# Kernel tuning notes

Hardware: AMD Instinct MI355X
Metric: run time of the kernel (lower is better)

The kernel has to match this reference:

```python
import jax, jax.numpy as jnp
import numpy as np

B, T, N, D = 64, 12, 207, 128
H, ORDER = 8, 2
HID = 2 * D  # mlp_ratio = 2


def _ln(x, g, b, eps=1e-5):
    m = x.mean(-1, keepdims=True)
    v = ((x - m) ** 2).mean(-1, keepdims=True)
    return (x - m) * jax.lax.rsqrt(v + eps) * g + b


def _l2norm(t, eps=1e-12):
    # matches torch.nn.functional.normalize(dim=-1)
    n = jnp.sqrt((t * t).sum(-1, keepdims=True))
    return t / jnp.maximum(n, eps)


def _fast_attn(q, k, v):
    # q, k, v: (B2, L, H, Dh); Performer-style linear attention from FastAttentionLayer.fast_attention
    q = _l2norm(q)
    k = _l2norm(k)
    L = q.shape[1]
    kvs = jnp.einsum('blhm,blhd->bhmd', k, v)
    num = jnp.einsum('bnhm,bhmd->bnhd', q, kvs) + L * v
    ks_sum = k.sum(axis=1)  # (B2, H, Dh)
    den = jnp.einsum('bnhm,bhm->bnh', q, ks_sum)[..., None] + L
    return num / jnp.maximum(den, 1e-5)


def _fast_layer(x, qkv_w, out_w, out_b):
    # x: (B, T, N, D). qkv_bias=False (mask arg), kernel=3 -> out_proj: Linear(2D, D)
    b, t, n, d = x.shape
    dh = d // H
    qkv = x @ qkv_w.T  # (B, T, N, 3D)
    q, k, v = jnp.split(qkv, 3, axis=-1)
    # spatial pass: attend over the N nodes for each (b, t)
    out_s = _fast_attn(q.reshape(b * t, n, H, dh),
                       k.reshape(b * t, n, H, dh),
                       v.reshape(b * t, n, H, dh)).reshape(b, t, n, d)
    # temporal pass: attend over the T steps for each (b, n)
    qt = q.transpose(0, 2, 1, 3).reshape(b * n, t, H, dh)
    kt = k.transpose(0, 2, 1, 3).reshape(b * n, t, H, dh)
    vt = v.transpose(0, 2, 1, 3).reshape(b * n, t, H, dh)
    out_t = _fast_attn(qt, kt, vt).reshape(b, n, t, d).transpose(0, 2, 1, 3)
    return jnp.concatenate([out_s, out_t], -1) @ out_w.T + out_b


def _forward(x, graph, qkv_w, out_w, out_b, pw_w, pw_b,
             fc1_w, fc1_b, fc2_w, fc2_b, ln1_g, ln1_b, ln2_g, ln2_b):
    # GraphPropagate: x_list = [x, graph @ x, ...] (Ks = ORDER hops)
    xs = [x]
    xk = x
    for _ in range(ORDER - 1):
        xk = jnp.einsum('thi,btij->bthj', graph, xk)
        xs.append(xk)
    # per-hop fast attention + zero-init pointwise branch, summed over hops
    agg = jnp.zeros_like(x)
    for i in range(ORDER):
        agg = agg + _fast_layer(xs[i], qkv_w[i], out_w[i], out_b[i]) + xs[i] @ pw_w[i].T + pw_b[i]
    h = _ln(x + agg, ln1_g, ln1_b)
    ff = jax.nn.relu(h @ fc1_w.T + fc1_b) @ fc2_w.T + fc2_b
    return _ln(h + ff, ln2_g, ln2_b)


def setup_inputs() -> dict:
    key = jax.random.key(0)
    ks = jax.random.split(key, 8)
    s = 0.02
    return {
        'x': jax.random.normal(ks[0], (B, T, N, D), jnp.float32),
        'graph': jax.random.uniform(ks[1], (T, N, N), jnp.float32) / N,
        'qkv_w': jax.random.normal(ks[2], (ORDER, 3 * D, D), jnp.float32) * s,
        'out_w': jax.random.normal(ks[3], (ORDER, D, 2 * D), jnp.float32) * s,
        'out_b': jnp.zeros((ORDER, D), jnp.float32),
        'pw_w': jax.random.normal(ks[4], (ORDER, D, D), jnp.float32) * s,
        'pw_b': jnp.zeros((ORDER, D), jnp.float32),
        'fc1_w': jax.random.normal(ks[5], (HID, D), jnp.float32) * s,
        'fc1_b': jnp.zeros((HID,), jnp.float32),
        'fc2_w': jax.random.normal(ks[6], (D, HID), jnp.float32) * s,
        'fc2_b': jnp.zeros((D,), jnp.float32),
        'ln1_g': jnp.ones((D,), jnp.float32),
        'ln1_b': jnp.zeros((D,), jnp.float32),
        'ln2_g': jnp.ones((D,), jnp.float32),
        'ln2_b': jnp.zeros((D,), jnp.float32),
    }


def reference(x, graph, qkv_w, out_w, out_b, pw_w, pw_b,
              fc1_w, fc1_b, fc2_w, fc2_b, ln1_g, ln1_b, ln2_g, ln2_b):
    return _forward(x, graph, qkv_w, out_w, out_b, pw_w, pw_b,
                    fc1_w, fc1_b, fc2_w, fc2_b, ln1_g, ln1_b, ln2_g, ln2_b)
```

## Files before the change

kernel.cpp:

```cpp
#include <hip/hip_runtime.h>
#include <hip/hip_bf16.h>

#define BB 64
#define TT 12
#define NN 207
#define DD 128
#define HH 8
#define DH 16
#define MROWS (BB*TT*NN)
#define KPAD 224
#define AW 768
#define CHB 32
#define CROWS (CHB*TT*NN)

typedef __bf16 bf16x8 __attribute__((ext_vector_type(8)));
typedef __bf16 bf16x4 __attribute__((ext_vector_type(4)));
typedef float  f32x4  __attribute__((ext_vector_type(4)));

__device__ inline float  b2f(__bf16 v){ return (float)v; }
__device__ inline __bf16 f2b(float v){ return (__bf16)v; }
__device__ inline bf16x8 ldfrag(const __bf16* p){ return *reinterpret_cast<const bf16x8*>(p); }

__device__ inline void gload_lds16(const __bf16* g, __bf16* l){
    __builtin_amdgcn_global_load_lds(
        (const __attribute__((address_space(1))) void*)(g),
        (__attribute__((address_space(3))) void*)(l), 16, 0, 0);
}
__device__ inline int swz(int r){ return (r ^ (r>>2)) & 3; }

__global__ __launch_bounds__(256) void xcopy_kernel(const float* __restrict__ x, __bf16* __restrict__ abuf)
{
    int nt = gridDim.x*256;
    for (int gIdx = blockIdx.x*256 + threadIdx.x; gIdx < MROWS*16; gIdx += nt) {
        int row = gIdx >> 4, c8 = (gIdx & 15)*8;
        const float* s = x + (size_t)row*DD + c8;
        f32x4 a = *reinterpret_cast<const f32x4*>(s);
        f32x4 b = *reinterpret_cast<const f32x4*>(s+4);
        bf16x8 r;
        #pragma unroll
        for (int i=0;i<4;i++){ r[i] = f2b(a[i]); r[i+4] = f2b(b[i]); }
        *reinterpret_cast<bf16x8*>(abuf + (size_t)row*AW + c8) = r;
    }
}

__global__ __launch_bounds__(256) void prep_misc_kernel(
    const float* __restrict__ graph, const float* __restrict__ qkv_w,
    const float* __restrict__ out_w, const float* __restrict__ out_b,
    const float* __restrict__ pw_w,  const float* __restrict__ pw_b,
    const float* __restrict__ fc1_w, const float* __restrict__ fc2_w,
    __bf16* __restrict__ gpad, __bf16* __restrict__ qkv_wb, __bf16* __restrict__ wcomb,
    __bf16* __restrict__ fc1_wb, __bf16* __restrict__ fc2_wb, float* __restrict__ bias_comb)
{
    int nt = gridDim.x*256;
    int tid = blockIdx.x*256 + threadIdx.x;
    for (int i = tid; i < TT*NN*KPAD; i += nt) {
        int k = i % KPAD, r = i / KPAD;
        gpad[i] = (k < NN) ? f2b(graph[(size_t)r*NN + k]) : f2b(0.f);
    }
    for (int i = tid; i < 2*3*DD*DD; i += nt) qkv_wb[i] = f2b(qkv_w[i]);
    for (int i = tid; i < DD*AW; i += nt) {
        int c = i / AW, j = i % AW;
        float v;
        if      (j < 128) v = pw_w[c*128 + j];
        else if (j < 256) v = pw_w[128*128 + c*128 + (j-128)];
        else if (j < 512) v = out_w[c*256 + (j-256)];
        else              v = out_w[128*256 + c*256 + (j-512)];
        wcomb[i] = f2b(v);
    }
    for (int i = tid; i < 2*DD*DD; i += nt) fc1_wb[i] = f2b(fc1_w[i]);
    for (int i = tid; i < 2*DD*DD; i += nt) fc2_wb[i] = f2b(fc2_w[i]);
    for (int i = tid; i < DD; i += nt)
        bias_comb[i] = pw_b[i] + pw_b[128+i] + out_b[i] + out_b[128+i];
}

__global__ __launch_bounds__(256) void propagate_kernel(const __bf16* __restrict__ gp,
    __bf16* __restrict__ abuf)
{
    int bt   = blockIdx.x;
    int t    = bt % TT;
    int tile = blockIdx.y;
    int lane = threadIdx.x & 63, w = threadIdx.x >> 6;
    int lhi = lane >> 4, llo = lane & 15;
    __shared__ __attribute__((aligned(16))) __bf16 XT[DD][40];
    const __bf16* xbt  = abuf + (size_t)bt*NN*AW;
    const __bf16* grow = gp + (size_t)t*NN*KPAD;
    int rowbase = tile*64 + w*16;
    f32x4 acc[8];
    #pragma unroll
    for (int i=0;i<8;i++) acc[i] = (f32x4){0.f,0.f,0.f,0.f};
    int arow = rowbase + llo; if (arow > NN-1) arow = NN-1;
    for (int k0=0; k0<KPAD; k0+=32) {
        __syncthreads();
        for (int kl = (threadIdx.x>>7); kl < 32; kl += 2) {
            int kk = k0 + kl, c = threadIdx.x & 127;
            XT[c][kl] = (kk < NN) ? xbt[(size_t)kk*AW + c] : f2b(0.f);
        }
        __syncthreads();
        bf16x8 a = ldfrag(grow + (size_t)arow*KPAD + k0 + lhi*8);
        #pragma unroll
        for (int cf=0;cf<8;cf++){
            bf16x8 b = *reinterpret_cast<const bf16x8*>(&XT[cf*16+llo][lhi*8]);
            acc[cf] = __builtin_amdgcn_mfma_f32_16x16x32_bf16(a, b, acc[cf], 0,0,0);
        }
    }
    #pragma unroll
    for (int e=0;e<4;e++){
        int row = rowbase + lhi*4 + e;
        if (row < NN) {
            #pragma unroll
            for (int cf=0;cf<8;cf++)
                abuf[((size_t)bt*NN + row)*AW + DD + cf*16 + llo] = f2b(acc[cf][e]);
        }
    }
}

template<int MODE, bool RELU>
__global__ __launch_bounds__(512) void gemm_kernel(const __bf16* __restrict__ A, size_t lda,
    const __bf16* __restrict__ W, const float* __restrict__ bias,
    void* out, size_t ldc, int K, int mend,
    const __bf16* __restrict__ resid, size_t ldr,
    const float* __restrict__ lng, const float* __restrict__ lnb)
{
    __shared__ __attribute__((aligned(16))) __bf16 lds[3][12288];
    int w = threadIdx.x >> 6, lane = threadIdx.x & 63;
    int lhi = lane >> 4, llo = lane & 15;
    size_t row0 = (size_t)blockIdx.x*256;
    int col0 = blockIdx.y*128;
    int nt = K >> 5;

    int sA0 = (w*2+0)*64 + lane, sA1 = (w*2+1)*64 + lane, sW = w*64 + lane;
    int rA0 = sA0>>2, uA0 = sA0&3, rA1 = sA1>>2, uA1 = sA1&3, rW = sW>>2, uW = sW&3;
    long gr0 = (long)row0 + rA0; if (gr0 >= mend) gr0 = mend-1;
    long gr1 = (long)row0 + rA1; if (gr1 >= mend) gr1 = mend-1;
    const __bf16* gA0 = A + (size_t)gr0*lda + ((uA0 ^ swz(rA0))<<3);
    const __bf16* gA1 = A + (size_t)gr1*lda + ((uA1 ^ swz(rA1))<<3);
    const __bf16* gW  = W + (size_t)(col0 + rW)*K + ((uW ^ swz(rW))<<3);
    __bf16* base0 = &lds[0][0];

    int aoff[2], woff[8];
    #pragma unroll
    for (int rt=0;rt<2;rt++){
        int rl = w*32 + rt*16 + llo;
        aoff[rt] = rl*32 + ((lhi ^ swz(rl))<<3);
    }
    #pragma unroll
    for (int cf=0;cf<8;cf++){
        int wr = cf*16 + llo;
        woff[cf] = 8192 + wr*32 + ((lhi ^ swz(wr))<<3);
    }

    f32x4 acc[2][8];
    #pragma unroll
    for (int i=0;i<2;i++)
        #pragma unroll
        for (int j=0;j<8;j++) acc[i][j] = (f32x4){0.f,0.f,0.f,0.f};

    #define STAGE(buf, tt) { int k0 = (tt)<<5; __bf16* Lw = base0 + (buf)*12288;           \
        gload_lds16(gA0 + k0, Lw + (w*2+0)*512);                                           \
        gload_lds16(gA1 + k0, Lw + (w*2+1)*512);                                           \
        gload_lds16(gW  + k0, Lw + 8192 + w*512); }

    STAGE(0,0); STAGE(1,1); STAGE(2,2);

    int cur = 0;
    for (int t = 0; t < nt; ++t) {
        if (t <= nt-3)      asm volatile("s_waitcnt vmcnt(6)" ::: "memory");
        else if (t == nt-2) asm volatile("s_waitcnt vmcnt(3)" ::: "memory");
        else                asm volatile("s_waitcnt vmcnt(0)" ::: "memory");
        __builtin_amdgcn_s_barrier();
        __builtin_amdgcn_sched_barrier(0);
        const __bf16* Lb = base0 + cur*12288;
        bf16x8 a[2], b[8];
        #pragma unroll
        for (int rt=0;rt<2;rt++) a[rt] = *reinterpret_cast<const bf16x8*>(&Lb[aoff[rt]]);
        #pragma unroll
        for (int cf=0;cf<8;cf++)  b[cf] = *reinterpret_cast<const bf16x8*>(&Lb[woff[cf]]);
        asm volatile("s_waitcnt lgkmcnt(0)" ::: "memory");
        __builtin_amdgcn_sched_barrier(0);
        __builtin_amdgcn_s_barrier();
        if (t+3 < nt) STAGE(cur, t+3);
        #pragma unroll
        for (int rt=0;rt<2;rt++)
            #pragma unroll
            for (int cf=0;cf<8;cf++)
                acc[rt][cf] = __builtin_amdgcn_mfma_f32_16x16x32_bf16(a[rt], b[cf], acc[rt][cf], 0,0,0);
        cur = (cur == 2) ? 0 : cur + 1;
    }
    #undef STAGE

    float bv[8];
    #pragma unroll
    for (int cf=0;cf<8;cf++) bv[cf] = bias ? bias[col0 + cf*16 + llo] : 0.f;

    if (MODE == 0) {
        #pragma unroll
        for (int rt=0;rt<2;rt++) {
            #pragma unroll
            for (int e=0;e<4;e++) {
                size_t row = row0 + (size_t)w*32 + rt*16 + lhi*4 + e;
                if ((long)row >= mend) continue;
                #pragma unroll
                for (int cf=0;cf<8;cf++) {
                    float v = acc[rt][cf][e] + bv[cf];
                    if (RELU) v = fmaxf(v, 0.f);
                    ((__bf16*)out)[row*ldc + col0 + cf*16 + llo] = f2b(v);
                }
            }
        }
    } else {
        float g8[8], b8[8];
        #pragma unroll
        for (int cf=0;cf<8;cf++){ int c = cf*16 + llo; g8[cf] = lng[c]; b8[cf] = lnb[c]; }
        #pragma unroll
        for (int rt=0;rt<2;rt++) {
            #pragma unroll
            for (int e=0;e<4;e++) {
                size_t row = row0 + (size_t)w*32 + rt*16 + lhi*4 + e;
                if ((long)row >= mend) continue;
                float vals[8], s = 0.f, ss = 0.f;
                #pragma unroll
                for (int cf=0;cf<8;cf++) {
                    int c = cf*16 + llo;
                    float r = b2f(resid[row*ldr + c]);
                    float v = acc[rt][cf][e] + bv[cf] + r;
                    vals[cf] = v; s += v; ss += v*v;
                }
                #pragma unroll
                for (int o=1;o<16;o<<=1){ s += __shfl_xor(s,o,64); ss += __shfl_xor(ss,o,64); }
                float mean = s * (1.f/DD);
                float var  = ss * (1.f/DD) - mean*mean;
                float rs   = rsqrtf(var + 1e-5f);
                #pragma unroll
                for (int cf=0;cf<8;cf++) {
                    float v = (vals[cf]-mean)*rs*g8[cf] + b8[cf];
                    size_t idx = row*ldc + cf*16 + llo;
                    if (MODE == 3) ((__bf16*)out)[idx] = f2b(v);
                    else           ((float*)out)[idx]  = v;
                }
            }
        }
    }
}

template<bool RELU>
__global__ __launch_bounds__(256) void sgemm_k128(const __bf16* __restrict__ A, size_t lda,
    const __bf16* __restrict__ W, const float* __restrict__ bias,
    __bf16* __restrict__ out, size_t ldc, int ngroups)
{
    __shared__ __attribute__((aligned(16))) __bf16 lds[12][2048];
    int w = threadIdx.x >> 6, lane = threadIdx.x & 63;
    int lhi = lane >> 4, llo = lane & 15;
    int col0 = blockIdx.y*128;

    bf16x8 wf[4][8];
    #pragma unroll
    for (int ks=0;ks<4;ks++)
        #pragma unroll
        for (int cf=0;cf<8;cf++)
            wf[ks][cf] = ldfrag(W + (size_t)(col0 + cf*16 + llo)*128 + ks*32 + lhi*8);

    f32x4 bvv[8];
    #pragma unroll
    for (int cf=0;cf<8;cf++){
        if (bias) bvv[cf] = *reinterpret_cast<const f32x4*>(bias + col0 + cf*16 + lhi*4);
        else      bvv[cf] = (f32x4){0.f,0.f,0.f,0.f};
    }

    size_t gsrc[4];
    #pragma unroll
    for (int j=0;j<4;j++){
        int r = j*4 + lhi;
        int u = llo ^ r;
        gsrc[j] = (size_t)r*lda + (size_t)u*8;
    }
    int aoff[4];
    #pragma unroll
    for (int ks=0;ks<4;ks++) aoff[ks] = llo*128 + (((ks<<2)|lhi) ^ llo)*8;

    int gw = blockIdx.x*4 + w, stride = gridDim.x*4;
    int n = (gw < ngroups) ? ((ngroups-1-gw)/stride + 1) : 0;
    __bf16* slab0 = &lds[w*3][0];

    #define SSTAGE(i) { size_t rbase = (size_t)(gw + (size_t)(i)*stride)*16*lda;           \
        __bf16* L = slab0 + ((i)%3)*2048;                                                  \
        gload_lds16(A + rbase + gsrc[0], L);                                               \
        gload_lds16(A + rbase + gsrc[1], L + 512);                                         \
        gload_lds16(A + rbase + gsrc[2], L + 1024);                                        \
        gload_lds16(A + rbase + gsrc[3], L + 1536); }

    if (n > 0) SSTAGE(0);
    if (n > 1) SSTAGE(1);

    for (int i = 0; i < n; ++i) {
        int kept = ((i+1 < n) ? 4 : 0) + ((i >= 2) ? 16 : i*8);
        if      (kept >= 20) asm volatile("s_waitcnt vmcnt(20)" ::: "memory");
        else if (kept == 16) asm volatile("s_waitcnt vmcnt(16)" ::: "memory");
        else if (kept == 12) asm volatile("s_waitcnt vmcnt(12)" ::: "memory");
        else if (kept == 8)  asm volatile("s_waitcnt vmcnt(8)"  ::: "memory");
        else if (kept == 4)  asm volatile("s_waitcnt vmcnt(4)"  ::: "memory");
        else                 asm volatile("s_waitcnt vmcnt(0)"  ::: "memory");

        const __bf16* Ls = slab0 + (i%3)*2048;
        bf16x8 a[4];
        #pragma unroll
        for (int ks=0;ks<4;ks++) a[ks] = *reinterpret_cast<const bf16x8*>(&Ls[aoff[ks]]);

        if (i+2 < n) SSTAGE(i+2);

        f32x4 acc[8];
        #pragma unroll
        for (int cf=0;cf<8;cf++) acc[cf] = (f32x4){0.f,0.f,0.f,0.f};
        #pragma unroll
        for (int ks=0;ks<4;ks++)
            #pragma unroll
            for (int cf=0;cf<8;cf++)
                acc[cf] = __builtin_amdgcn_mfma_f32_16x16x32_bf16(wf[ks][cf], a[ks], acc[cf], 0,0,0);

        size_t grow = (size_t)(gw + (size_t)i*stride)*16 + llo;
        #pragma unroll
        for (int cf=0;cf<8;cf++){
            bf16x4 o;
            #pragma unroll
            for (int e=0;e<4;e++){
                float v = acc[cf][e] + bvv[cf][e];
                if (RELU) v = fmaxf(v, 0.f);
                o[e] = f2b(v);
            }
            *reinterpret_cast<bf16x4*>(out + grow*ldc + col0 + cf*16 + lhi*4) = o;
        }
    }
    #undef SSTAGE
}

#define ACH 32
__global__ __launch_bounds__(256) void attn_s_kernel(const __bf16* __restrict__ qkv,
                                                     __bf16* __restrict__ outp)
{
    int bt = blockIdx.x, g = blockIdx.y;
    const __bf16* base = qkv + (size_t)bt*NN*384 + g*32;
    __shared__ __attribute__((aligned(16))) __bf16 qbuf[224][40];
    __shared__ __attribute__((aligned(16))) __bf16 vbuf[224][40];
    __shared__ __attribute__((aligned(16))) __bf16 kbuf[ACH][40];
    __shared__ float flk[4][16][17];
    __shared__ float fls[4][16];
    int tid = threadIdx.x;
    int wave = tid >> 6, lane = tid & 63;
    int h2 = tid >> 7;
    int dd = tid & 15;
    int oct = ((tid >> 4) & 3) | ((wave & 1) << 2);
    float kvs_col[16]; float ks = 0.f;
    #pragma unroll
    for (int m=0;m<16;m++) kvs_col[m] = 0.f;

    for (int c0 = 0; c0 < NN; c0 += ACH) {
        __syncthreads();
        for (int i = tid; i < ACH*12; i += 256) {
            int r = i/12, u = i%12, seg = u>>2, uu = u&3;
            int nn = c0 + r;
            bf16x8 v8 = (bf16x8){};
            if (nn < NN) v8 = *reinterpret_cast<const bf16x8*>(base + (size_t)nn*384 + seg*128 + uu*8);
            if      (seg == 0) *reinterpret_cast<bf16x8*>(&qbuf[nn][uu*8]) = v8;
            else if (seg == 1) *reinterpret_cast<bf16x8*>(&kbuf[r][uu*8])  = v8;
            else               *reinterpret_cast<bf16x8*>(&vbuf[nn][uu*8]) = v8;
        }
        __syncthreads();
        #pragma unroll
        for (int j=0;j<4;j++){
            int r = oct + 8*j; int nn = c0 + r;
            if (nn >= NN) continue;
            bf16x8 k0 = *reinterpret_cast<const bf16x8*>(&kbuf[r][h2*16]);
            bf16x8 k1 = *reinterpret_cast<const bf16x8*>(&kbuf[r][h2*16+8]);
            float sk = 0.f;
            #pragma unroll
            for (int m=0;m<8;m++){
                float a0=b2f(k0[m]), a1=b2f(k1[m]); sk += a0*a0 + a1*a1;
            }
            float iv = 1.f/fmaxf(sqrtf(sk), 1e-12f);
            float vv  = b2f(vbuf[nn][h2*16+dd]);
            float kdd = b2f(kbuf[r][h2*16+dd]);
            float t2 = iv*vv;
            #pragma unroll
            for (int m=0;m<8;m++){
                kvs_col[m]   += b2f(k0[m])*t2;
                kvs_col[m+8] += b2f(k1[m])*t2;
            }
            ks += kdd*iv;
        }
    }
    #pragma unroll
    for (int m=0;m<16;m++){
        kvs_col[m] += __shfl_xor(kvs_col[m], 16, 64);
        kvs_col[m] += __shfl_xor(kvs_col[m], 32, 64);
    }
    ks += __shfl_xor(ks, 16, 64);
    ks += __shfl_xor(ks, 32, 64);
    if (lane < 16){
        #pragma unroll
        for (int m=0;m<16;m++) flk[wave][m][lane] = kvs_col[m];
        fls[wave][lane] = ks;
    }
    __syncthreads();
    float ksr[16];
    #pragma unroll
    for (int m=0;m<16;m++){
        kvs_col[m] += flk[wave^1][m][dd];
        ksr[m] = fls[h2*2][m] + fls[h2*2+1][m];
    }

    for (int nn = oct; nn < NN; nn += 8) {
        bf16x8 q0 = *reinterpret_cast<const bf16x8*>(&qbuf[nn][h2*16]);
        bf16x8 q1 = *reinterpret_cast<const bf16x8*>(&qbuf[nn][h2*16+8]);
        float sq = 0.f, num = 0.f, den = 0.f;
        #pragma unroll
        for (int m=0;m<8;m++){
            float qm0 = b2f(q0[m]), qm1 = b2f(q1[m]);
            sq  += qm0*qm0 + qm1*qm1;
            num += qm0*kvs_col[m] + qm1*kvs_col[m+8];
            den += qm0*ksr[m]     + qm1*ksr[m+8];
        }
        float iq = 1.f/fmaxf(sqrtf(sq), 1e-12f);
        float vv = b2f(vbuf[nn][h2*16+dd]);
        float o = (num*iq + (float)NN*vv) / fmaxf(den*iq + (float)NN, 1e-5f);
        outp[((size_t)bt*NN + nn)*AW + g*32 + h2*16 + dd] = f2b(o);
    }
}

__global__ __launch_bounds__(256) void attn_t_kernel(const __bf16* __restrict__ qkv,
                                                     __bf16* __restrict__ outp)
{
    int b = blockIdx.x;
    int nn0 = blockIdx.y * 2;
    __shared__ __attribute__((aligned(16))) __bf16 rows[TT][2][384];
    __shared__ float invq[2][TT][8], invk2[2][TT][8];
    int tid = threadIdx.x;
    for (int i = tid; i < TT*2*48; i += 256) {
        int t = i / 96, rem = i % 96;
        int nl = rem / 48, g = rem % 48;
        int nn = nn0 + nl;
        bf16x8 v8 = (bf16x8){};
        if (nn < NN) v8 = *reinterpret_cast<const bf16x8*>(qkv + ((size_t)(b*TT+t)*NN + nn)*384 + g*8);
        *reinterpret_cast<bf16x8*>(&rows[t][nl][g*8]) = v8;
    }
    __syncthreads();
    if (tid < 192) {
        int hh = tid & 7, t = (tid >> 3) % TT, nl = tid / 96;
        bf16x8 q0 = *reinterpret_cast<const bf16x8*>(&rows[t][nl][hh*16]);
        bf16x8 q1 = *reinterpret_cast<const bf16x8*>(&rows[t][nl][hh*16+8]);
        bf16x8 k0 = *reinterpret_cast<const bf16x8*>(&rows[t][nl][128+hh*16]);
        bf16x8 k1 = *reinterpret_cast<const bf16x8*>(&rows[t][nl][128+hh*16+8]);
        float sq = 0.f, sk = 0.f;
        #pragma unroll
        for (int m=0;m<8;m++){
            float a0=b2f(q0[m]), a1=b2f(q1[m]); sq += a0*a0 + a1*a1;
            float c0v=b2f(k0[m]), c1=b2f(k1[m]); sk += c0v*c0v + c1*c1;
        }
        invq[nl][t][hh]  = 1.f/fmaxf(sqrtf(sq), 1e-12f);
        invk2[nl][t][hh] = 1.f/fmaxf(sqrtf(sk), 1e-12f);
    }
    __syncthreads();
    int dd = tid & 15, h = (tid >> 4) & 7, nl = tid >> 7;
    int nn = nn0 + nl;
    float kvs_col[16], ksum[16];
    #pragma unroll
    for (int m=0;m<16;m++){ kvs_col[m]=0.f; ksum[m]=0.f; }
    #pragma unroll
    for (int t=0;t<TT;t++){
        float iv = invk2[nl][t][h];
        bf16x8 k0 = *reinterpret_cast<const bf16x8*>(&rows[t][nl][128+h*16]);
        bf16x8 k1 = *reinterpret_cast<const bf16x8*>(&rows[t][nl][128+h*16+8]);
        float vv = b2f(rows[t][nl][256+h*16+dd]);
        float t2 = iv*vv;
        #pragma unroll
        for (int m=0;m<8;m++){
            float km0 = b2f(k0[m]), km1 = b2f(k1[m]);
            kvs_col[m]   += km0*t2;  ksum[m]   += km0*iv;
            kvs_col[m+8] += km1*t2;  ksum[m+8] += km1*iv;
        }
    }
    #pragma unroll
    for (int t=0;t<TT;t++){
        float iq = invq[nl][t][h];
        bf16x8 q0 = *reinterpret_cast<const bf16x8*>(&rows[t][nl][h*16]);
        bf16x8 q1 = *reinterpret_cast<const bf16x8*>(&rows[t][nl][h*16+8]);
        float num = 0.f, den = 0.f;
        #pragma unroll
        for (int m=0;m<8;m++){
            float qm0 = b2f(q0[m]), qm1 = b2f(q1[m]);
            num += qm0*kvs_col[m]  + qm1*kvs_col[m+8];
            den += qm0*ksum[m]     + qm1*ksum[m+8];
        }
        float vv = b2f(rows[t][nl][256+h*16+dd]);
        float o = (num*iq + (float)TT*vv) / fmaxf(den*iq + (float)TT, 1e-5f);
        if (nn < NN)
            outp[((size_t)(b*TT+t)*NN + nn)*AW + h*16 + dd] = f2b(o);
    }
}

extern "C" void kernel_launch(void* const* d_in, const int* in_sizes, int n_in,
                              void* d_out, int out_size, void* d_ws, size_t ws_size,
                              hipStream_t stream)
{
    const float* x     = (const float*)d_in[0];
    const float* graph = (const float*)d_in[1];
    const float* qkv_w = (const float*)d_in[2];
    const float* out_w = (const float*)d_in[3];
    const float* out_b = (const float*)d_in[4];
    const float* pw_w  = (const float*)d_in[5];
    const float* pw_b  = (const float*)d_in[6];
    const float* fc1_w = (const float*)d_in[7];
    const float* fc1_b = (const float*)d_in[8];
    const float* fc2_w = (const float*)d_in[9];
    const float* fc2_b = (const float*)d_in[10];
    const float* ln1g  = (const float*)d_in[11];
    const float* ln1b  = (const float*)d_in[12];
    const float* ln2g  = (const float*)d_in[13];
    const float* ln2b  = (const float*)d_in[14];
    (void)in_sizes; (void)n_in; (void)out_size; (void)ws_size;

    char* ws = (char*)d_ws;
    size_t off = 0;
    __bf16* abuf = (__bf16*)(ws + off); off += (size_t)MROWS*AW*2;
    __bf16* qkvc = (__bf16*)(ws + off); off += (size_t)CROWS*3*DD*2;
    __bf16* gpad = (__bf16*)(ws + off); off += (size_t)TT*NN*KPAD*2;
    __bf16* qkv_wb = (__bf16*)(ws + off); off += (size_t)2*3*DD*DD*2;
    __bf16* wcomb  = (__bf16*)(ws + off); off += (size_t)DD*AW*2;
    __bf16* fc1_wb = (__bf16*)(ws + off); off += (size_t)2*DD*DD*2;
    __bf16* fc2_wb = (__bf16*)(ws + off); off += (size_t)2*DD*DD*2;
    float*  bias_comb = (float*)(ws + off); off += DD*4;

    dim3 blk(256), blk512(512);

    xcopy_kernel<<<dim3(4096), blk, 0, stream>>>(x, abuf);
    prep_misc_kernel<<<dim3(1024), blk, 0, stream>>>(graph, qkv_w, out_w, out_b, pw_w, pw_b,
        fc1_w, fc2_w, gpad, qkv_wb, wcomb, fc1_wb, fc2_wb, bias_comb);
    propagate_kernel<<<dim3(BB*TT, 4), blk, 0, stream>>>(gpad, abuf);

    for (int hop = 0; hop < 2; ++hop) {
        for (int c = 0; c < BB/CHB; ++c) {
            size_t rowoff = (size_t)c*CROWS;
            sgemm_k128<false><<<dim3(170, 3), blk, 0, stream>>>(
                abuf + rowoff*AW + hop*DD, (size_t)AW, qkv_wb + (size_t)hop*3*DD*DD, nullptr,
                qkvc, (size_t)(3*DD), CROWS/16);
            attn_s_kernel<<<dim3(CHB*TT, 4), blk, 0, stream>>>(
                qkvc, abuf + rowoff*AW + 256 + hop*256);
            attn_t_kernel<<<dim3(CHB, (NN+1)/2), blk, 0, stream>>>(
                qkvc, abuf + rowoff*AW + 384 + hop*256);
        }
    }

    gemm_kernel<3,false><<<dim3(MROWS/256, 1), blk512, 0, stream>>>(
        abuf, (size_t)AW, wcomb, bias_comb, (void*)abuf, (size_t)AW, AW, MROWS,
        abuf, (size_t)AW, ln1g, ln1b);
    sgemm_k128<true><<<dim3(256, 2), blk, 0, stream>>>(
        abuf, (size_t)AW, fc1_wb, fc1_b, abuf + 256, (size_t)AW, MROWS/16);
    gemm_kernel<4,false><<<dim3(MROWS/256, 1), blk512, 0, stream>>>(
        abuf + 256, (size_t)AW, fc2_wb, fc2_b, d_out, (size_t)DD, 2*DD, MROWS,
        abuf, (size_t)AW, ln2g, ln2b);
}
```

Measured before the change: 840.8 us.

## Fuse FFN into one register kernel, merge attention kernels, swizzle propagate LDS

Three separate changes. The fc1 GEMM, ReLU, fc2 GEMM, residual add and LayerNorm2 now run in one kernel that keeps the hidden activation in registers and shuffles it between lanes, so the bf16 hidden tensor no longer makes a round trip through global memory. The spatial and temporal attention kernels are merged into one launch that splits its blocks by index, cutting launch count and letting the two passes overlap. The XT tile in the propagate kernel gets an XOR swizzle to cut LDS bank conflicts. The FFN kernel reads weight fragments straight from global memory with no LDS staging, which could limit its throughput.

```diff
diff --git a/kernel.cpp b/kernel.cpp
--- a/kernel.cpp
+++ b/kernel.cpp
@@ -27,6 +27,7 @@
         (__attribute__((address_space(3))) void*)(l), 16, 0, 0);
 }
 __device__ inline int swz(int r){ return (r ^ (r>>2)) & 3; }
+__device__ inline int pkey(int c){ return (c + (c>>2)) & 3; }
 
 __global__ __launch_bounds__(256) void xcopy_kernel(const float* __restrict__ x, __bf16* __restrict__ abuf)
 {
@@ -93,13 +94,15 @@
         __syncthreads();
         for (int kl = (threadIdx.x>>7); kl < 32; kl += 2) {
             int kk = k0 + kl, c = threadIdx.x & 127;
-            XT[c][kl] = (kk < NN) ? xbt[(size_t)kk*AW + c] : f2b(0.f);
+            __bf16 xb = (kk < NN) ? xbt[(size_t)kk*AW + c] : f2b(0.f);
+            XT[c][(((kl>>3) ^ pkey(c))<<3) | (kl&7)] = xb;
         }
         __syncthreads();
         bf16x8 a = ldfrag(grow + (size_t)arow*KPAD + k0 + lhi*8);
         #pragma unroll
         for (int cf=0;cf<8;cf++){
-            bf16x8 b = *reinterpret_cast<const bf16x8*>(&XT[cf*16+llo][lhi*8]);
+            int row = cf*16+llo;
+            bf16x8 b = *reinterpret_cast<const bf16x8*>(&XT[row][(lhi ^ pkey(row))<<3]);
             acc[cf] = __builtin_amdgcn_mfma_f32_16x16x32_bf16(a, b, acc[cf], 0,0,0);
         }
     }
@@ -233,9 +236,7 @@
                 #pragma unroll
                 for (int cf=0;cf<8;cf++) {
                     float v = (vals[cf]-mean)*rs*g8[cf] + b8[cf];
-                    size_t idx = row*ldc + cf*16 + llo;
-                    if (MODE == 3) ((__bf16*)out)[idx] = f2b(v);
-                    else           ((float*)out)[idx]  = v;
+                    ((__bf16*)out)[row*ldc + cf*16 + llo] = f2b(v);
                 }
             }
         }
@@ -332,167 +333,263 @@
     #undef SSTAGE
 }
 
+__global__ __launch_bounds__(256) void ffn_reg_kernel(const __bf16* __restrict__ h,
+    const __bf16* __restrict__ w1, const float* __restrict__ b1,
+    const __bf16* __restrict__ w2, const float* __restrict__ b2,
+    const float* __restrict__ lng, const float* __restrict__ lnb,
+    float* __restrict__ dout)
+{
+    int wv = threadIdx.x >> 6, lane = threadIdx.x & 63;
+    int lhi = lane >> 4, llo = lane & 15;
+    int gw = blockIdx.x*4 + wv, stride = gridDim.x*4;
+    int srcA = ((lhi & 1)*2)*16 + llo;
+    int srcB = srcA + 16;
+    bool hiSel = (lhi >= 2);
+
+    f32x4 gv[2], bt2[2], b2v[2];
+    #pragma unroll
+    for (int cf2=0;cf2<2;cf2++){
+        gv[cf2] = (f32x4){0,0,0,0}; bt2[cf2] = gv[cf2]; b2v[cf2] = gv[cf2];
+    }
+
+    for (int g = gw; g < MROWS/16; g += stride) {
+        size_t row = (size_t)g*16 + llo;
+        const __bf16* hrow = h + row*AW;
+
+        bf16x8 a[4];
+        #pragma unroll
+        for (int ks=0;ks<4;ks++) a[ks] = ldfrag(hrow + ks*32 + lhi*8);
+        bf16x4 hres[8];
+        #pragma unroll
+        for (int cf=0;cf<8;cf++)
+            hres[cf] = *reinterpret_cast<const bf16x4*>(hrow + cf*16 + lhi*4);
+
+        f32x4 acc2[8];
+        #pragma unroll
+        for (int cf=0;cf<8;cf++) acc2[cf] = (f32x4){0.f,0.f,0.f,0.f};
+
+        #pragma unroll
+        for (int ks2=0;ks2<8;ks2++){
+            f32x4 accA = (f32x4){0,0,0,0}, accB = (f32x4){0,0,0,0};
+            #pragma unroll
+            for (int ks=0;ks<4;ks++){
+                bf16x8 wA = ldfrag(w1 + (size_t)((2*ks2+0)*16 + llo)*128 + ks*32 + lhi*8);
+                bf16x8 wB = ldfrag(w1 + (size_t)((2*ks2+1)*16 + llo)*128 + ks*32 + lhi*8);
+                accA = __builtin_amdgcn_mfma_f32_16x16x32_bf16(wA, a[ks], accA, 0,0,0);
+                accB = __builtin_amdgcn_mfma_f32_16x16x32_bf16(wB, a[ks], accB, 0,0,0);
+            }
+            f32x4 bA = *reinterpret_cast<const f32x4*>(b1 + (2*ks2+0)*16 + lhi*4);
+            f32x4 bB = *reinterpret_cast<const f32x4*>(b1 + (2*ks2+1)*16 + lhi*4);
+            union { bf16x4 v; int i2[2]; } pA, pB;
+            #pragma unroll
+            for (int e=0;e<4;e++){
+                pA.v[e] = f2b(fmaxf(accA[e] + bA[e], 0.f));
+                pB.v[e] = f2b(fmaxf(accB[e] + bB[e], 0.f));
+            }
+            int A0x = __shfl(pA.i2[0], srcA, 64), A0y = __shfl(pA.i2[1], srcA, 64);
+            int A1x = __shfl(pA.i2[0], srcB, 64), A1y = __shfl(pA.i2[1], srcB, 64);
+            int B0x = __shfl(pB.i2[0], srcA, 64), B0y = __shfl(pB.i2[1], srcA, 64);
+            int B1x = __shfl(pB.i2[0], srcB, 64), B1y = __shfl(pB.i2[1], srcB, 64);
+            union { bf16x8 v; int i4[4]; } fb;
+            fb.i4[0] = hiSel ? B0x : A0x;
+            fb.i4[1] = hiSel ? B0y : A0y;
+            fb.i4[2] = hiSel ? B1x : A1x;
+            fb.i4[3] = hiSel ? B1y : A1y;
+            #pragma unroll
+            for (int cf=0;cf<8;cf++){
+                bf16x8 w2f = ldfrag(w2 + (size_t)(cf*16 + llo)*256 + ks2*32 + lhi*8);
+                acc2[cf] = __builtin_amdgcn_mfma_f32_16x16x32_bf16(w2f, fb.v, acc2[cf], 0,0,0);
+            }
+        }
+
+        float s = 0.f, ss = 0.f;
+        #pragma unroll
+        for (int cf=0;cf<8;cf++){
+            f32x4 bv = *reinterpret_cast<const f32x4*>(b2 + cf*16 + lhi*4);
+            #pragma unroll
+            for (int e=0;e<4;e++){
+                float v = acc2[cf][e] + bv[e] + b2f(hres[cf][e]);
+                acc2[cf][e] = v; s += v; ss += v*v;
+            }
+        }
+        s  += __shfl_xor(s,16,64);  s  += __shfl_xor(s,32,64);
+        ss += __shfl_xor(ss,16,64); ss += __shfl_xor(ss,32,64);
+        float mean = s*(1.f/DD), var = ss*(1.f/DD)-mean*mean, rs = rsqrtf(var+1e-5f);
+        #pragma unroll
+        for (int cf=0;cf<8;cf++){
+            f32x4 gvv = *reinterpret_cast<const f32x4*>(lng + cf*16 + lhi*4);
+            f32x4 btv = *reinterpret_cast<const f32x4*>(lnb + cf*16 + lhi*4);
+            f32x4 o;
+            #pragma unroll
+            for (int e=0;e<4;e++) o[e] = (acc2[cf][e]-mean)*rs*gvv[e] + btv[e];
+            *reinterpret_cast<f32x4*>(dout + row*DD + cf*16 + lhi*4) = o;
+        }
+    }
+}
+
 #define ACH 32
-__global__ __launch_bounds__(256) void attn_s_kernel(const __bf16* __restrict__ qkv,
-                                                     __bf16* __restrict__ outp)
-{
-    int bt = blockIdx.x, g = blockIdx.y;
-    const __bf16* base = qkv + (size_t)bt*NN*384 + g*32;
-    __shared__ __attribute__((aligned(16))) __bf16 qbuf[224][40];
-    __shared__ __attribute__((aligned(16))) __bf16 vbuf[224][40];
-    __shared__ __attribute__((aligned(16))) __bf16 kbuf[ACH][40];
-    __shared__ float flk[4][16][17];
-    __shared__ float fls[4][16];
+#define SBLKS (CHB*TT*4)
+__global__ __launch_bounds__(256) void attn_st_kernel(const __bf16* __restrict__ qkv,
+    __bf16* __restrict__ outs, __bf16* __restrict__ outt)
+{
+    __shared__ __attribute__((aligned(16))) char smem[44032];
     int tid = threadIdx.x;
-    int wave = tid >> 6, lane = tid & 63;
-    int h2 = tid >> 7;
-    int dd = tid & 15;
-    int oct = ((tid >> 4) & 3) | ((wave & 1) << 2);
-    float kvs_col[16]; float ks = 0.f;
-    #pragma unroll
-    for (int m=0;m<16;m++) kvs_col[m] = 0.f;
-
-    for (int c0 = 0; c0 < NN; c0 += ACH) {
+    int bx = blockIdx.x;
+
+    if (bx < SBLKS) {
+        int bt = bx >> 2, g = bx & 3;
+        const __bf16* base = qkv + (size_t)bt*NN*384 + g*32;
+        __bf16 (*qbuf)[40] = (__bf16(*)[40])(smem);
+        __bf16 (*vbuf)[40] = (__bf16(*)[40])(smem + 17920);
+        __bf16 (*kbuf)[40] = (__bf16(*)[40])(smem + 35840);
+        float (*flk)[16][17] = (float(*)[16][17])(smem + 38400);
+        float (*fls)[16]     = (float(*)[16])(smem + 42752);
+        int wave = tid >> 6, lane = tid & 63;
+        int h2 = tid >> 7;
+        int dd = tid & 15;
+        int oct = ((tid >> 4) & 3) | ((wave & 1) << 2);
+        float kvs_col[16]; float ks = 0.f;
+        #pragma unroll
+        for (int m=0;m<16;m++) kvs_col[m] = 0.f;
+
+        for (int c0 = 0; c0 < NN; c0 += ACH) {
+            __syncthreads();
+            for (int i = tid; i < ACH*12; i += 256) {
+                int r = i/12, u = i%12, seg = u>>2, uu = u&3;
+                int nn = c0 + r;
+                bf16x8 v8 = (bf16x8){};
+                if (nn < NN) v8 = *reinterpret_cast<const bf16x8*>(base + (size_t)nn*384 + seg*128 + uu*8);
+                if      (seg == 0) *reinterpret_cast<bf16x8*>(&qbuf[nn][uu*8]) = v8;
+                else if (seg == 1) *reinterpret_cast<bf16x8*>(&kbuf[r][uu*8])  = v8;
+                else               *reinterpret_cast<bf16x8*>(&vbuf[nn][uu*8]) = v8;
+            }
+            __syncthreads();
+            #pragma unroll
+            for (int j=0;j<4;j++){
+                int r = oct + 8*j; int nn = c0 + r;
+                if (nn >= NN) continue;
+                bf16x8 k0 = *reinterpret_cast<const bf16x8*>(&kbuf[r][h2*16]);
+                bf16x8 k1 = *reinterpret_cast<const bf16x8*>(&kbuf[r][h2*16+8]);
+                float sk = 0.f;
+                #pragma unroll
+                for (int m=0;m<8;m++){
+                    float a0=b2f(k0[m]), a1=b2f(k1[m]); sk += a0*a0 + a1*a1;
+                }
+                float iv = 1.f/fmaxf(sqrtf(sk), 1e-12f);
+                float vv  = b2f(vbuf[nn][h2*16+dd]);
+                float kdd = b2f(kbuf[r][h2*16+dd]);
+                float t2 = iv*vv;
+                #pragma unroll
+                for (int m=0;m<8;m++){
+                    kvs_col[m]   += b2f(k0[m])*t2;
+                    kvs_col[m+8] += b2f(k1[m])*t2;
+                }
+                ks += kdd*iv;
+            }
+        }
+        #pragma unroll
+        for (int m=0;m<16;m++){
+            kvs_col[m] += __shfl_xor(kvs_col[m], 16, 64);
+            kvs_col[m] += __shfl_xor(kvs_col[m], 32, 64);
+        }
+        ks += __shfl_xor(ks, 16, 64);
+        ks += __shfl_xor(ks, 32, 64);
+        if (lane < 16){
+            #pragma unroll
+            for (int m=0;m<16;m++) flk[wave][m][lane] = kvs_col[m];
+            fls[wave][lane] = ks;
+        }
         __syncthreads();
-        for (int i = tid; i < ACH*12; i += 256) {
-            int r = i/12, u = i%12, seg = u>>2, uu = u&3;
-            int nn = c0 + r;
+        float ksr[16];
+        #pragma unroll
+        for (int m=0;m<16;m++){
+            kvs_col[m] += flk[wave^1][m][dd];
+            ksr[m] = fls[h2*2][m] + fls[h2*2+1][m];
+        }
+        for (int nn = oct; nn < NN; nn += 8) {
+            bf16x8 q0 = *reinterpret_cast<const bf16x8*>(&qbuf[nn][h2*16]);
+            bf16x8 q1 = *reinterpret_cast<const bf16x8*>(&qbuf[nn][h2*16+8]);
+            float sq = 0.f, num = 0.f, den = 0.f;
+            #pragma unroll
+            for (int m=0;m<8;m++){
+                float qm0 = b2f(q0[m]), qm1 = b2f(q1[m]);
+                sq  += qm0*qm0 + qm1*qm1;
+                num += qm0*kvs_col[m] + qm1*kvs_col[m+8];
+                den += qm0*ksr[m]     + qm1*ksr[m+8];
+            }
+            float iq = 1.f/fmaxf(sqrtf(sq), 1e-12f);
+            float vv = b2f(vbuf[nn][h2*16+dd]);
+            float o = (num*iq + (float)NN*vv) / fmaxf(den*iq + (float)NN, 1e-5f);
+            outs[((size_t)bt*NN + nn)*AW + g*32 + h2*16 + dd] = f2b(o);
+        }
+    } else {
+        int tix = bx - SBLKS;
+        int b = tix / 104;
+        int nn0 = (tix % 104) * 2;
+        __bf16 (*rows)[2][384] = (__bf16(*)[2][384])(smem);
+        float (*invq)[TT][8]  = (float(*)[TT][8])(smem + 18432);
+        float (*invk2)[TT][8] = (float(*)[TT][8])(smem + 19200);
+        for (int i = tid; i < TT*2*48; i += 256) {
+            int t = i / 96, rem = i % 96;
+            int nl = rem / 48, g = rem % 48;
+            int nn = nn0 + nl;
             bf16x8 v8 = (bf16x8){};
-            if (nn < NN) v8 = *reinterpret_cast<const bf16x8*>(base + (size_t)nn*384 + seg*128 + uu*8);
-            if      (seg == 0) *reinterpret_cast<bf16x8*>(&qbuf[nn][uu*8]) = v8;
-            else if (seg == 1) *reinterpret_cast<bf16x8*>(&kbuf[r][uu*8])  = v8;
-            else               *reinterpret_cast<bf16x8*>(&vbuf[nn][uu*8]) = v8;
+            if (nn < NN) v8 = *reinterpret_cast<const bf16x8*>(qkv + ((size_t)(b*TT+t)*NN + nn)*384 + g*8);
+            *reinterpret_cast<bf16x8*>(&rows[t][nl][g*8]) = v8;
         }
         __syncthreads();
-        #pragma unroll
-        for (int j=0;j<4;j++){
-            int r = oct + 8*j; int nn = c0 + r;
-            if (nn >= NN) continue;
-            bf16x8 k0 = *reinterpret_cast<const bf16x8*>(&kbuf[r][h2*16]);
-            bf16x8 k1 = *reinterpret_cast<const bf16x8*>(&kbuf[r][h2*16+8]);
-            float sk = 0.f;
+        if (tid < 192) {
+            int hh = tid & 7, t = (tid >> 3) % TT, nl = tid / 96;
+            bf16x8 q0 = *reinterpret_cast<const bf16x8*>(&rows[t][nl][hh*16]);
+            bf16x8 q1 = *reinterpret_cast<const bf16x8*>(&rows[t][nl][hh*16+8]);
+            bf16x8 k0 = *reinterpret_cast<const bf16x8*>(&rows[t][nl][128+hh*16]);
+            bf16x8 k1 = *reinterpret_cast<const bf16x8*>(&rows[t][nl][128+hh*16+8]);
+            float sq = 0.f, sk = 0.f;
             #pragma unroll
             for (int m=0;m<8;m++){
-                float a0=b2f(k0[m]), a1=b2f(k1[m]); sk += a0*a0 + a1*a1;
-            }
-            float iv = 1.f/fmaxf(sqrtf(sk), 1e-12f);
-            float vv  = b2f(vbuf[nn][h2*16+dd]);
-            float kdd = b2f(kbuf[r][h2*16+dd]);
+                float a0=b2f(q0[m]), a1=b2f(q1[m]); sq += a0*a0 + a1*a1;
+                float c0v=b2f(k0[m]), c1=b2f(k1[m]); sk += c0v*c0v + c1*c1;
+            }
+            invq[nl][t][hh]  = 1.f/fmaxf(sqrtf(sq), 1e-12f);
+            invk2[nl][t][hh] = 1.f/fmaxf(sqrtf(sk), 1e-12f);
+        }
+        __syncthreads();
+        int dd = tid & 15, h = (tid >> 4) & 7, nl = tid >> 7;
+        int nn = nn0 + nl;
+        float kvs_col[16], ksum[16];
+        #pragma unroll
+        for (int m=0;m<16;m++){ kvs_col[m]=0.f; ksum[m]=0.f; }
+        #pragma unroll
+        for (int t=0;t<TT;t++){
+            float iv = invk2[nl][t][h];
+            bf16x8 k0 = *reinterpret_cast<const bf16x8*>(&rows[t][nl][128+h*16]);
+            bf16x8 k1 = *reinterpret_cast<const bf16x8*>(&rows[t][nl][128+h*16+8]);
+            float vv = b2f(rows[t][nl][256+h*16+dd]);
             float t2 = iv*vv;
             #pragma unroll
             for (int m=0;m<8;m++){
-                kvs_col[m]   += b2f(k0[m])*t2;
-                kvs_col[m+8] += b2f(k1[m])*t2;
-            }
-            ks += kdd*iv;
-        }
-    }
-    #pragma unroll
-    for (int m=0;m<16;m++){
-        kvs_col[m] += __shfl_xor(kvs_col[m], 16, 64);
-        kvs_col[m] += __shfl_xor(kvs_col[m], 32, 64);
-    }
-    ks += __shfl_xor(ks, 16, 64);
-    ks += __shfl_xor(ks, 32, 64);
-    if (lane < 16){
-        #pragma unroll
-        for (int m=0;m<16;m++) flk[wave][m][lane] = kvs_col[m];
-        fls[wave][lane] = ks;
-    }
-    __syncthreads();
-    float ksr[16];
-    #pragma unroll
-    for (int m=0;m<16;m++){
-        kvs_col[m] += flk[wave^1][m][dd];
-        ksr[m] = fls[h2*2][m] + fls[h2*2+1][m];
-    }
-
-    for (int nn = oct; nn < NN; nn += 8) {
-        bf16x8 q0 = *reinterpret_cast<const bf16x8*>(&qbuf[nn][h2*16]);
-        bf16x8 q1 = *reinterpret_cast<const bf16x8*>(&qbuf[nn][h2*16+8]);
-        float sq = 0.f, num = 0.f, den = 0.f;
-        #pragma unroll
-        for (int m=0;m<8;m++){
-            float qm0 = b2f(q0[m]), qm1 = b2f(q1[m]);
-            sq  += qm0*qm0 + qm1*qm1;
-            num += qm0*kvs_col[m] + qm1*kvs_col[m+8];
-            den += qm0*ksr[m]     + qm1*ksr[m+8];
-        }
-        float iq = 1.f/fmaxf(sqrtf(sq), 1e-12f);
-        float vv = b2f(vbuf[nn][h2*16+dd]);
-        float o = (num*iq + (float)NN*vv) / fmaxf(den*iq + (float)NN, 1e-5f);
-        outp[((size_t)bt*NN + nn)*AW + g*32 + h2*16 + dd] = f2b(o);
-    }
-}
-
-__global__ __launch_bounds__(256) void attn_t_kernel(const __bf16* __restrict__ qkv,
-                                                     __bf16* __restrict__ outp)
-{
-    int b = blockIdx.x;
-    int nn0 = blockIdx.y * 2;
-    __shared__ __attribute__((aligned(16))) __bf16 rows[TT][2][384];
-    __shared__ float invq[2][TT][8], invk2[2][TT][8];
-    int tid = threadIdx.x;
-    for (int i = tid; i < TT*2*48; i += 256) {
-        int t = i / 96, rem = i % 96;
-        int nl = rem / 48, g = rem % 48;
-        int nn = nn0 + nl;
-        bf16x8 v8 = (bf16x8){};
-        if (nn < NN) v8 = *reinterpret_cast<const bf16x8*>(qkv + ((size_t)(b*TT+t)*NN + nn)*384 + g*8);
-        *reinterpret_cast<bf16x8*>(&rows[t][nl][g*8]) = v8;
-    }
-    __syncthreads();
-    if (tid < 192) {
-        int hh = tid & 7, t = (tid >> 3) % TT, nl = tid / 96;
-        bf16x8 q0 = *reinterpret_cast<const bf16x8*>(&rows[t][nl][hh*16]);
-        bf16x8 q1 = *reinterpret_cast<const bf16x8*>(&rows[t][nl][hh*16+8]);
-        bf16x8 k0 = *reinterpret_cast<const bf16x8*>(&rows[t][nl][128+hh*16]);
-        bf16x8 k1 = *reinterpret_cast<const bf16x8*>(&rows[t][nl][128+hh*16+8]);
-        float sq = 0.f, sk = 0.f;
-        #pragma unroll
-        for (int m=0;m<8;m++){
-            float a0=b2f(q0[m]), a1=b2f(q1[m]); sq += a0*a0 + a1*a1;
-            float c0v=b2f(k0[m]), c1=b2f(k1[m]); sk += c0v*c0v + c1*c1;
-        }
-        invq[nl][t][hh]  = 1.f/fmaxf(sqrtf(sq), 1e-12f);
-        invk2[nl][t][hh] = 1.f/fmaxf(sqrtf(sk), 1e-12f);
-    }
-    __syncthreads();
-    int dd = tid & 15, h = (tid >> 4) & 7, nl = tid >> 7;
-    int nn = nn0 + nl;
-    float kvs_col[16], ksum[16];
-    #pragma unroll
-    for (int m=0;m<16;m++){ kvs_col[m]=0.f; ksum[m]=0.f; }
-    #pragma unroll
-    for (int t=0;t<TT;t++){
-        float iv = invk2[nl][t][h];
-        bf16x8 k0 = *reinterpret_cast<const bf16x8*>(&rows[t][nl][128+h*16]);
-        bf16x8 k1 = *reinterpret_cast<const bf16x8*>(&rows[t][nl][128+h*16+8]);
-        float vv = b2f(rows[t][nl][256+h*16+dd]);
-        float t2 = iv*vv;
-        #pragma unroll
-        for (int m=0;m<8;m++){
-            float km0 = b2f(k0[m]), km1 = b2f(k1[m]);
-            kvs_col[m]   += km0*t2;  ksum[m]   += km0*iv;
-            kvs_col[m+8] += km1*t2;  ksum[m+8] += km1*iv;
-        }
-    }
-    #pragma unroll
-    for (int t=0;t<TT;t++){
-        float iq = invq[nl][t][h];
-        bf16x8 q0 = *reinterpret_cast<const bf16x8*>(&rows[t][nl][h*16]);
-        bf16x8 q1 = *reinterpret_cast<const bf16x8*>(&rows[t][nl][h*16+8]);
-        float num = 0.f, den = 0.f;
-        #pragma unroll
-        for (int m=0;m<8;m++){
-            float qm0 = b2f(q0[m]), qm1 = b2f(q1[m]);
-            num += qm0*kvs_col[m]  + qm1*kvs_col[m+8];
-            den += qm0*ksum[m]     + qm1*ksum[m+8];
-        }
-        float vv = b2f(rows[t][nl][256+h*16+dd]);
-        float o = (num*iq + (float)TT*vv) / fmaxf(den*iq + (float)TT, 1e-5f);
-        if (nn < NN)
-            outp[((size_t)(b*TT+t)*NN + nn)*AW + h*16 + dd] = f2b(o);
+                float km0 = b2f(k0[m]), km1 = b2f(k1[m]);
+                kvs_col[m]   += km0*t2;  ksum[m]   += km0*iv;
+                kvs_col[m+8] += km1*t2;  ksum[m+8] += km1*iv;
+            }
+        }
+        #pragma unroll
+        for (int t=0;t<TT;t++){
+            float iq = invq[nl][t][h];
+            bf16x8 q0 = *reinterpret_cast<const bf16x8*>(&rows[t][nl][h*16]);
+            bf16x8 q1 = *reinterpret_cast<const bf16x8*>(&rows[t][nl][h*16+8]);
+            float num = 0.f, den = 0.f;
+            #pragma unroll
+            for (int m=0;m<8;m++){
+                float qm0 = b2f(q0[m]), qm1 = b2f(q1[m]);
+                num += qm0*kvs_col[m]  + qm1*kvs_col[m+8];
+                den += qm0*ksum[m]     + qm1*ksum[m+8];
+            }
+            float vv = b2f(rows[t][nl][256+h*16+dd]);
+            float o = (num*iq + (float)TT*vv) / fmaxf(den*iq + (float)TT, 1e-5f);
+            if (nn < NN)
+                outt[((size_t)(b*TT+t)*NN + nn)*AW + h*16 + dd] = f2b(o);
+        }
     }
 }
 
@@ -541,19 +638,14 @@
             sgemm_k128<false><<<dim3(170, 3), blk, 0, stream>>>(
                 abuf + rowoff*AW + hop*DD, (size_t)AW, qkv_wb + (size_t)hop*3*DD*DD, nullptr,
                 qkvc, (size_t)(3*DD), CROWS/16);
-            attn_s_kernel<<<dim3(CHB*TT, 4), blk, 0, stream>>>(
-                qkvc, abuf + rowoff*AW + 256 + hop*256);
-            attn_t_kernel<<<dim3(CHB, (NN+1)/2), blk, 0, stream>>>(
-                qkvc, abuf + rowoff*AW + 384 + hop*256);
+            attn_st_kernel<<<dim3(SBLKS + CHB*104), blk, 0, stream>>>(
+                qkvc, abuf + rowoff*AW + 256 + hop*256, abuf + rowoff*AW + 384 + hop*256);
         }
     }
 
     gemm_kernel<3,false><<<dim3(MROWS/256, 1), blk512, 0, stream>>>(
         abuf, (size_t)AW, wcomb, bias_comb, (void*)abuf, (size_t)AW, AW, MROWS,
         abuf, (size_t)AW, ln1g, ln1b);
-    sgemm_k128<true><<<dim3(256, 2), blk, 0, stream>>>(
-        abuf, (size_t)AW, fc1_wb, fc1_b, abuf + 256, (size_t)AW, MROWS/16);
-    gemm_kernel<4,false><<<dim3(MROWS/256, 1), blk512, 0, stream>>>(
-        abuf + 256, (size_t)AW, fc2_wb, fc2_b, d_out, (size_t)DD, 2*DD, MROWS,
-        abuf, (size_t)AW, ln2g, ln2b);
-}
+    ffn_reg_kernel<<<dim3(621), blk, 0, stream>>>(
+        abuf, fc1_wb, fc1_b, fc2_wb, fc2_b, ln2g, ln2b, (float*)d_out);
+}
```

Measured after the change: 1.102 ms. 1.31x slower.
